# Kernel optimization log

Hardware: AMD Instinct MI355X
Metric: run time of the kernel (lower is better)

The kernel has to match this reference:

```python
import jax, jax.numpy as jnp
import numpy as np

B, N, DIM = 2, 2048, 1024
HEADS, DIM_HEAD = 16, 64
INNER = HEADS * DIM_HEAD  # 1024
SCALE = DIM_HEAD ** -0.5


def setup_inputs() -> dict:
    key = jax.random.key(0)
    ks = jax.random.split(key, 6)
    s = lambda k, shape, fan: jax.random.normal(k, shape, jnp.float32) * (fan ** -0.5)
    return {
        "x": jax.random.normal(ks[0], (B, N, DIM), jnp.float32),
        "similarity": jax.random.normal(ks[1], (B, N), jnp.float32),
        "Wq": s(ks[2], (DIM, INNER), DIM),
        "Wkv": s(ks[3], (DIM, 2 * INNER), DIM),
        "Wo": s(ks[4], (INNER, DIM), INNER),
        "bo": jnp.zeros((DIM,), jnp.float32),
    }


def reference(x, similarity, Wq, Wkv, Wo, bo):
    b, n, _ = x.shape
    h, d = HEADS, DIM_HEAD
    # projections (context = x, self-attention)
    q = (x @ Wq).reshape(b, n, h, d).transpose(0, 2, 1, 3)        # b h n d
    kv = x @ Wkv                                                   # b n 2*inner
    k, v = jnp.split(kv, 2, axis=-1)
    k = k.reshape(b, n, h, d).transpose(0, 2, 1, 3)
    v = v.reshape(b, n, h, d).transpose(0, 2, 1, 3)
    dots = jnp.einsum('bhid,bhjd->bhij', q, k) * SCALE             # b h n n
    # similarity [b,n] -> broadcast as per-query row bias [b,1,n,1]
    dots = dots + similarity[:, None, :, None]
    attn = jax.nn.softmax(dots, axis=-1)
    out = jnp.einsum('bhij,bhjd->bhid', attn, v)                   # b h n d
    out = out.transpose(0, 2, 1, 3).reshape(b, n, h * d)           # b n inner
    return out @ Wo + bo
```

## Files before the change

kernel.cpp:

```cpp
#include <hip/hip_runtime.h>


typedef __attribute__((ext_vector_type(8))) short short8;
typedef __attribute__((ext_vector_type(4))) float float4_;
typedef __attribute__((ext_vector_type(16))) float floatx16;
typedef __attribute__((ext_vector_type(4))) unsigned short ushort4_;

#define MFMA(a, b, c) __builtin_amdgcn_mfma_f32_16x16x32_bf16((a), (b), (c), 0, 0, 0)
#define MFMA32(a, b, c) __builtin_amdgcn_mfma_f32_32x32x16_bf16((a), (b), (c), 0, 0, 0)

static __device__ __forceinline__ unsigned short f2bf(float f) {
    union { float f; unsigned int u; } v; v.f = f;
    unsigned int r = v.u + 0x7FFFu + ((v.u >> 16) & 1u);
    return (unsigned short)(r >> 16);
}

static __device__ __forceinline__ void gld16(const void* g, void* l) {
    __builtin_amdgcn_global_load_lds(
        (__attribute__((address_space(1))) void*)(g),
        (__attribute__((address_space(3))) void*)(l), 16, 0, 0);
}

__global__ __launch_bounds__(256) void prep(
    const float* __restrict__ X, const float* __restrict__ Wq,
    const float* __restrict__ Wkv, const float* __restrict__ Wo,
    unsigned short* __restrict__ xb, unsigned short* __restrict__ Wt,
    unsigned short* __restrict__ Wot)
{
    const int bid = blockIdx.x, t = threadIdx.x;
    if (bid >= 1024) {
        const int b = bid - 1024;
        const float4_* src = (const float4_*)X;
        ushort4_* dst = (ushort4_*)xb;
        #pragma unroll
        for (int g = 0; g < 8; ++g) {
            const int idx = b * 2048 + g * 256 + t;
            float4_ v = src[idx];
            ushort4_ o;
            o[0] = f2bf(v[0]); o[1] = f2bf(v[1]);
            o[2] = f2bf(v[2]); o[3] = f2bf(v[3]);
            dst[idx] = o;
        }
        return;
    }
    __shared__ float tile[64][65];
    const float* src; unsigned short* dst; int N, kt, nt, drow0;
    if (bid < 256)      { src = Wq;  N = 1024; kt = bid & 15;       nt = bid >> 4;       dst = Wt;  drow0 = nt * 64; }
    else if (bid < 768) { src = Wkv; N = 2048; kt = (bid-256) & 15; nt = (bid-256) >> 4; dst = Wt;  drow0 = 1024 + nt * 64; }
    else                { src = Wo;  N = 1024; kt = (bid-768) & 15; nt = (bid-768) >> 4; dst = Wot; drow0 = nt * 64; }
    const int k0 = kt * 64, n0 = nt * 64;
    const int r0 = t >> 6, c = t & 63;
    #pragma unroll
    for (int i = 0; i < 16; ++i) {
        const int r = i * 4 + r0;
        tile[r][c] = src[(size_t)(k0 + r) * N + n0 + c];
    }
    __syncthreads();
    #pragma unroll
    for (int i = 0; i < 16; ++i) {
        const int rn = i * 4 + r0;
        dst[(size_t)(drow0 + rn) * 1024 + k0 + c] = f2bf(tile[c][rn]);
    }
}

__global__ __launch_bounds__(256) void qkv_gemm2(
    const unsigned short* __restrict__ xb, const unsigned short* __restrict__ Wt,
    unsigned short* __restrict__ q_ws, unsigned short* __restrict__ k_ws,
    unsigned short* __restrict__ vt_ws)
{
    __shared__ unsigned short As[128 * 64];
    __shared__ unsigned short Bs[128 * 64];
    const int t = threadIdx.x, wave = t >> 6, lane = t & 63;
    const int L = lane & 15, quad = lane >> 4;
    const int mb = blockIdx.x / 24, nb = blockIdx.x % 24;
    const int m0 = mb * 128, n0 = nb * 128;
    const int wr = wave >> 1, wc = wave & 1;

    float4_ z = {0.f, 0.f, 0.f, 0.f};
    float4_ acc[4][4];
    #pragma unroll
    for (int i = 0; i < 4; ++i)
        #pragma unroll
        for (int j = 0; j < 4; ++j) acc[i][j] = z;

    const unsigned short* gA[4]; const unsigned short* gB[4];
    unsigned short* lA[4]; unsigned short* lB[4];
    #pragma unroll
    for (int j = 0; j < 4; ++j) {
        const int cid = wave * 256 + j * 64 + lane;
        const int row = cid >> 3, pc = cid & 7;
        const int lch = pc ^ (row & 7);
        gA[j] = xb + (size_t)(m0 + row) * 1024 + lch * 8;
        gB[j] = Wt + (size_t)(n0 + row) * 1024 + lch * 8;
        lA[j] = As + wave * 2048 + j * 512;
        lB[j] = Bs + wave * 2048 + j * 512;
    }

    for (int kc = 0; kc < 1024; kc += 64) {
        #pragma unroll
        for (int j = 0; j < 4; ++j) {
            gld16(gA[j] + kc, lA[j]);
            gld16(gB[j] + kc, lB[j]);
        }
        __syncthreads();
        #pragma unroll
        for (int ks = 0; ks < 2; ++ks) {
            short8 af[4], bfr[4];
            #pragma unroll
            for (int mt = 0; mt < 4; ++mt) {
                const int rl = wr * 64 + mt * 16 + L;
                af[mt] = *(const short8*)(As + rl * 64 + (((ks * 4 + quad) ^ (L & 7)) << 3));
            }
            #pragma unroll
            for (int nt = 0; nt < 4; ++nt) {
                const int rl = wc * 64 + nt * 16 + L;
                bfr[nt] = *(const short8*)(Bs + rl * 64 + (((ks * 4 + quad) ^ (L & 7)) << 3));
            }
            #pragma unroll
            for (int mt = 0; mt < 4; ++mt)
                #pragma unroll
                for (int nt = 0; nt < 4; ++nt)
                    acc[mt][nt] = MFMA(af[mt], bfr[nt], acc[mt][nt]);
        }
        __syncthreads();
    }

    const int b = m0 >> 11;
    const int type = n0 >> 10;
    #pragma unroll
    for (int mt = 0; mt < 4; ++mt) {
        const int m = (m0 & 2047) + wr * 64 + mt * 16 + quad * 4;
        #pragma unroll
        for (int nt = 0; nt < 4; ++nt) {
            const int cl = (n0 & 1023) + wc * 64 + nt * 16 + L;
            const int h = cl >> 6, d = cl & 63;
            float4_ v = acc[mt][nt];
            if (type == 0) {
                unsigned short* p = q_ws + ((size_t)(b * 16 + h) * 2048 + m) * 64 + d;
                #pragma unroll
                for (int r = 0; r < 4; ++r) p[(size_t)r * 64] = f2bf(v[r] * 0.18033688011f);
            } else if (type == 1) {
                unsigned short* p = k_ws + ((size_t)(b * 16 + h) * 2048 + m) * 64 + d;
                #pragma unroll
                for (int r = 0; r < 4; ++r) p[(size_t)r * 64] = f2bf(v[r]);
            } else {
                ushort4_ pk;
                pk[0] = f2bf(v[0]); pk[1] = f2bf(v[1]);
                pk[2] = f2bf(v[2]); pk[3] = f2bf(v[3]);
                *(ushort4_*)(vt_ws + ((size_t)(b * 16 + h) * 64 + d) * 2048 + m) = pk;
            }
        }
    }
}

__global__ __launch_bounds__(256) void attn_fwd2(
    const unsigned short* __restrict__ q_ws,
    const unsigned short* __restrict__ k_ws,
    const unsigned short* __restrict__ vt_ws,
    unsigned short* __restrict__ o2)
{
    __shared__ unsigned short k_lds[2][64 * 64];
    __shared__ unsigned short v_lds[2][64 * 64];
    __shared__ unsigned short p_lds[128 * 64];
    const int t = threadIdx.x, wave = t >> 6, lane = t & 63;
    const int l32 = lane & 31, hi = lane >> 5;
    const int bh = blockIdx.x >> 4, qb = blockIdx.x & 15;

    const unsigned short* Kp = k_ws + (size_t)bh * 2048 * 64;
    const unsigned short* Vt = vt_ws + (size_t)bh * 64 * 2048;

    const unsigned short* Qp = q_ws + ((size_t)bh * 2048 + qb * 128 + wave * 32 + l32) * 64;
    short8 qf[4];
    #pragma unroll
    for (int s = 0; s < 4; ++s) qf[s] = *(const short8*)(Qp + hi * 8 + s * 16);

    const int c0 = wave * 64 + lane;
    const int kr0 = c0 >> 3, kl0 = (c0 & 7) ^ (kr0 & 7);
    const int kr1 = kr0 + 32, kl1 = kl0;
    const unsigned short* ks0 = Kp + (size_t)kr0 * 64 + kl0 * 8;
    const unsigned short* ks1 = Kp + (size_t)kr1 * 64 + kl1 * 8;
    const unsigned short* vs0 = Vt + (size_t)kr0 * 2048 + kl0 * 8;
    const unsigned short* vs1 = Vt + (size_t)kr1 * 2048 + kl1 * 8;
    const int dst0 = wave * 512, dst1 = 2048 + wave * 512;

    floatx16 o0 = {0.f}, o1 = {0.f};
    #pragma unroll
    for (int r = 0; r < 16; ++r) { o0[r] = 0.f; o1[r] = 0.f; }
    float lsum[16];
    #pragma unroll
    for (int r = 0; r < 16; ++r) lsum[r] = 0.f;

    gld16(ks0, k_lds[0] + dst0); gld16(ks1, k_lds[0] + dst1);
    gld16(vs0, v_lds[0] + dst0); gld16(vs1, v_lds[0] + dst1);
    __syncthreads();

    const int prow = wave * 32 + l32;
    const int myrow[4] = {0, 1, 2, 3};

    for (int j0 = 0; j0 < 2048; j0 += 64) {
        const int p = (j0 >> 6) & 1;
        if (j0 + 64 < 2048) {
            const int np = p ^ 1;
            gld16(ks0 + (j0 + 64) * 64, k_lds[np] + dst0);
            gld16(ks1 + (j0 + 64) * 64, k_lds[np] + dst1);
            gld16(vs0 + (j0 + 64), v_lds[np] + dst0);
            gld16(vs1 + (j0 + 64), v_lds[np] + dst1);
        }
        const unsigned short* kb = k_lds[p];
        const unsigned short* vb = v_lds[p];

        floatx16 s0 = o0, s1 = o0;
        #pragma unroll
        for (int r = 0; r < 16; ++r) { s0[r] = 0.f; s1[r] = 0.f; }
        #pragma unroll
        for (int s = 0; s < 4; ++s) {
            const int lch = hi + 2 * s;
            short8 k0 = *(const short8*)(kb + l32 * 64 + ((lch ^ (l32 & 7)) << 3));
            short8 k1 = *(const short8*)(kb + (32 + l32) * 64 + ((lch ^ (l32 & 7)) << 3));
            s0 = MFMA32(qf[s], k0, s0);
            s1 = MFMA32(qf[s], k1, s1);
        }

        #pragma unroll
        for (int r = 0; r < 16; ++r) {
            const int row = wave * 32 + (r & 3) + 8 * (r >> 2) + 4 * hi;
            float p0 = __builtin_amdgcn_exp2f(s0[r]);
            float p1 = __builtin_amdgcn_exp2f(s1[r]);
            lsum[r] += p0 + p1;
            union { float f; unsigned int u; } cv0, cv1;
            cv0.f = p0; cv1.f = p1;
            const int ch0 = (l32 >> 3) ^ (row & 7);
            const int ch1 = (4 + (l32 >> 3)) ^ (row & 7);
            p_lds[row * 64 + ch0 * 8 + (l32 & 7)] = (unsigned short)(cv0.u >> 16);
            p_lds[row * 64 + ch1 * 8 + (l32 & 7)] = (unsigned short)(cv1.u >> 16);
        }

        #pragma unroll
        for (int s = 0; s < 4; ++s) {
            const int lch = hi + 2 * s;
            short8 pa = *(const short8*)(p_lds + prow * 64 + ((lch ^ (prow & 7)) << 3));
            short8 v0 = *(const short8*)(vb + l32 * 64 + ((lch ^ (l32 & 7)) << 3));
            short8 v1 = *(const short8*)(vb + (32 + l32) * 64 + ((lch ^ (l32 & 7)) << 3));
            o0 = MFMA32(pa, v0, o0);
            o1 = MFMA32(pa, v1, o1);
        }
        __syncthreads();
    }

    float inv[16];
    #pragma unroll
    for (int r = 0; r < 16; ++r) {
        float l = lsum[r];
        l += __shfl_xor(l, 1); l += __shfl_xor(l, 2);
        l += __shfl_xor(l, 4); l += __shfl_xor(l, 8);
        l += __shfl_xor(l, 16);
        inv[r] = 1.0f / l;
    }
    const int b = bh >> 4, h = bh & 15;
    unsigned short* ob = o2 + ((size_t)b * 2048 + qb * 128 + wave * 32) * 1024 + h * 64;
    #pragma unroll
    for (int r = 0; r < 16; ++r) {
        const int row = (r & 3) + 8 * (r >> 2) + 4 * hi;
        ob[(size_t)row * 1024 + l32]      = f2bf(o0[r] * inv[r]);
        ob[(size_t)row * 1024 + 32 + l32] = f2bf(o1[r] * inv[r]);
    }
}

__global__ __launch_bounds__(256) void out_gemm2(
    const unsigned short* __restrict__ o2, const unsigned short* __restrict__ Wot,
    const float* __restrict__ bo, float* __restrict__ Out)
{
    __shared__ unsigned short As[128 * 64];
    __shared__ unsigned short Bs[64 * 64];
    const int t = threadIdx.x, wave = t >> 6, lane = t & 63;
    const int L = lane & 15, quad = lane >> 4;
    const int mb = blockIdx.x >> 4, nb = blockIdx.x & 15;
    const int m0 = mb * 128, n0 = nb * 64;
    const int wr = wave >> 1, wc = wave & 1;

    float4_ z = {0.f, 0.f, 0.f, 0.f};
    float4_ acc[4][2];
    #pragma unroll
    for (int i = 0; i < 4; ++i)
        #pragma unroll
        for (int j = 0; j < 2; ++j) acc[i][j] = z;

    const unsigned short* gA[4]; unsigned short* lA[4];
    #pragma unroll
    for (int j = 0; j < 4; ++j) {
        const int cid = wave * 256 + j * 64 + lane;
        const int row = cid >> 3, pc = cid & 7;
        gA[j] = o2 + (size_t)(m0 + row) * 1024 + (pc ^ (row & 7)) * 8;
        lA[j] = As + wave * 2048 + j * 512;
    }
    const unsigned short* gB[2]; unsigned short* lB[2];
    #pragma unroll
    for (int j = 0; j < 2; ++j) {
        const int cid = wave * 128 + j * 64 + lane;
        const int row = cid >> 3, pc = cid & 7;
        gB[j] = Wot + (size_t)(n0 + row) * 1024 + (pc ^ (row & 7)) * 8;
        lB[j] = Bs + wave * 1024 + j * 512;
    }

    for (int kc = 0; kc < 1024; kc += 64) {
        #pragma unroll
        for (int j = 0; j < 4; ++j) gld16(gA[j] + kc, lA[j]);
        #pragma unroll
        for (int j = 0; j < 2; ++j) gld16(gB[j] + kc, lB[j]);
        __syncthreads();
        #pragma unroll
        for (int ks = 0; ks < 2; ++ks) {
            short8 af[4], bfr[2];
            #pragma unroll
            for (int mt = 0; mt < 4; ++mt) {
                const int rl = wr * 64 + mt * 16 + L;
                af[mt] = *(const short8*)(As + rl * 64 + (((ks * 4 + quad) ^ (L & 7)) << 3));
            }
            #pragma unroll
            for (int nt = 0; nt < 2; ++nt) {
                const int rl = wc * 32 + nt * 16 + L;
                bfr[nt] = *(const short8*)(Bs + rl * 64 + (((ks * 4 + quad) ^ (L & 7)) << 3));
            }
            #pragma unroll
            for (int mt = 0; mt < 4; ++mt)
                #pragma unroll
                for (int nt = 0; nt < 2; ++nt)
                    acc[mt][nt] = MFMA(af[mt], bfr[nt], acc[mt][nt]);
        }
        __syncthreads();
    }

    #pragma unroll
    for (int mt = 0; mt < 4; ++mt) {
        const int m = m0 + wr * 64 + mt * 16 + quad * 4;
        #pragma unroll
        for (int nt = 0; nt < 2; ++nt) {
            const int c = n0 + wc * 32 + nt * 16 + L;
            const float bias = bo[c];
            #pragma unroll
            for (int r = 0; r < 4; ++r)
                Out[(size_t)(m + r) * 1024 + c] = acc[mt][nt][r] + bias;
        }
    }
}

extern "C" void kernel_launch(void* const* d_in, const int* in_sizes, int n_in,
                              void* d_out, int out_size, void* d_ws, size_t ws_size,
                              hipStream_t stream) {
    const float* x   = (const float*)d_in[0];
    const float* Wq  = (const float*)d_in[2];
    const float* Wkv = (const float*)d_in[3];
    const float* Wo  = (const float*)d_in[4];
    const float* bo  = (const float*)d_in[5];
    float* out = (float*)d_out;

    char* ws = (char*)d_ws;
    const size_t MB = 1024 * 1024;
    unsigned short* xb   = (unsigned short*)(ws);
    unsigned short* o2   = xb;
    unsigned short* Wt   = (unsigned short*)(ws + 8 * MB);
    unsigned short* Wot  = (unsigned short*)(ws + 14 * MB);
    unsigned short* q_ws = (unsigned short*)(ws + 16 * MB);
    unsigned short* k_ws = (unsigned short*)(ws + 24 * MB);
    unsigned short* vt_ws= (unsigned short*)(ws + 32 * MB);

    prep<<<dim3(1536), dim3(256), 0, stream>>>(x, Wq, Wkv, Wo, xb, Wt, Wot);
    qkv_gemm2<<<dim3(768), dim3(256), 0, stream>>>(xb, Wt, q_ws, k_ws, vt_ws);
    attn_fwd2<<<dim3(512), dim3(256), 0, stream>>>(q_ws, k_ws, vt_ws, o2);
    out_gemm2<<<dim3(512), dim3(256), 0, stream>>>(o2, Wot, bo, out);
}
```

Before: 208.2 us.

## Keep attention probabilities in registers by transposing S MFMA operands

The QK^T MFMA now uses K as the A operand and Q as B, so each lane holds score values in an arrangement that can be packed straight into the bf16 A fragment of the PV MFMA. This removes the per-tile round trip of P through LDS (the scattered 16-bit stores and reloads) and reduces row sums to one scalar per lane. V reads become split 8-byte LDS loads that match the permuted key ordering, and row sums are exchanged through a small LDS array at the end. The risk is that the V fragment permutation must match the packed P layout exactly. The ls array is written and read across lanes without a barrier, which relies on lockstep execution within a wave.

Result: faster. 198.1 us (-4.9%).

```diff
diff --git a/kernel.cpp b/kernel.cpp
--- a/kernel.cpp
+++ b/kernel.cpp
@@ -5,6 +5,7 @@
 typedef __attribute__((ext_vector_type(4))) float float4_;
 typedef __attribute__((ext_vector_type(16))) float floatx16;
 typedef __attribute__((ext_vector_type(4))) unsigned short ushort4_;
+typedef __attribute__((ext_vector_type(4))) unsigned int uint4_;
 
 #define MFMA(a, b, c) __builtin_amdgcn_mfma_f32_16x16x32_bf16((a), (b), (c), 0, 0, 0)
 #define MFMA32(a, b, c) __builtin_amdgcn_mfma_f32_32x32x16_bf16((a), (b), (c), 0, 0, 0)
@@ -153,7 +154,7 @@
     }
 }
 
-__global__ __launch_bounds__(256) void attn_fwd2(
+__global__ __launch_bounds__(256) void attn_fwd3(
     const unsigned short* __restrict__ q_ws,
     const unsigned short* __restrict__ k_ws,
     const unsigned short* __restrict__ vt_ws,
@@ -161,7 +162,7 @@
 {
     __shared__ unsigned short k_lds[2][64 * 64];
     __shared__ unsigned short v_lds[2][64 * 64];
-    __shared__ unsigned short p_lds[128 * 64];
+    __shared__ float ls[4][32];
     const int t = threadIdx.x, wave = t >> 6, lane = t & 63;
     const int l32 = lane & 31, hi = lane >> 5;
     const int bh = blockIdx.x >> 4, qb = blockIdx.x & 15;
@@ -176,27 +177,23 @@
 
     const int c0 = wave * 64 + lane;
     const int kr0 = c0 >> 3, kl0 = (c0 & 7) ^ (kr0 & 7);
-    const int kr1 = kr0 + 32, kl1 = kl0;
+    const int kr1 = kr0 + 32;
     const unsigned short* ks0 = Kp + (size_t)kr0 * 64 + kl0 * 8;
-    const unsigned short* ks1 = Kp + (size_t)kr1 * 64 + kl1 * 8;
+    const unsigned short* ks1 = Kp + (size_t)kr1 * 64 + kl0 * 8;
     const unsigned short* vs0 = Vt + (size_t)kr0 * 2048 + kl0 * 8;
-    const unsigned short* vs1 = Vt + (size_t)kr1 * 2048 + kl1 * 8;
+    const unsigned short* vs1 = Vt + (size_t)kr1 * 2048 + kl0 * 8;
     const int dst0 = wave * 512, dst1 = 2048 + wave * 512;
 
-    floatx16 o0 = {0.f}, o1 = {0.f};
+    floatx16 o0, o1;
     #pragma unroll
     for (int r = 0; r < 16; ++r) { o0[r] = 0.f; o1[r] = 0.f; }
-    float lsum[16];
-    #pragma unroll
-    for (int r = 0; r < 16; ++r) lsum[r] = 0.f;
+    float lsum = 0.f;
 
     gld16(ks0, k_lds[0] + dst0); gld16(ks1, k_lds[0] + dst1);
     gld16(vs0, v_lds[0] + dst0); gld16(vs1, v_lds[0] + dst1);
     __syncthreads();
 
-    const int prow = wave * 32 + l32;
-    const int myrow[4] = {0, 1, 2, 3};
-
+    const int sw = l32 & 7;
     for (int j0 = 0; j0 < 2048; j0 += 64) {
         const int p = (j0 >> 6) & 1;
         if (j0 + 64 < 2048) {
@@ -209,53 +206,67 @@
         const unsigned short* kb = k_lds[p];
         const unsigned short* vb = v_lds[p];
 
-        floatx16 s0 = o0, s1 = o0;
+        floatx16 s0, s1;
         #pragma unroll
         for (int r = 0; r < 16; ++r) { s0[r] = 0.f; s1[r] = 0.f; }
         #pragma unroll
         for (int s = 0; s < 4; ++s) {
-            const int lch = hi + 2 * s;
-            short8 k0 = *(const short8*)(kb + l32 * 64 + ((lch ^ (l32 & 7)) << 3));
-            short8 k1 = *(const short8*)(kb + (32 + l32) * 64 + ((lch ^ (l32 & 7)) << 3));
-            s0 = MFMA32(qf[s], k0, s0);
-            s1 = MFMA32(qf[s], k1, s1);
-        }
-
-        #pragma unroll
-        for (int r = 0; r < 16; ++r) {
-            const int row = wave * 32 + (r & 3) + 8 * (r >> 2) + 4 * hi;
-            float p0 = __builtin_amdgcn_exp2f(s0[r]);
-            float p1 = __builtin_amdgcn_exp2f(s1[r]);
-            lsum[r] += p0 + p1;
-            union { float f; unsigned int u; } cv0, cv1;
-            cv0.f = p0; cv1.f = p1;
-            const int ch0 = (l32 >> 3) ^ (row & 7);
-            const int ch1 = (4 + (l32 >> 3)) ^ (row & 7);
-            p_lds[row * 64 + ch0 * 8 + (l32 & 7)] = (unsigned short)(cv0.u >> 16);
-            p_lds[row * 64 + ch1 * 8 + (l32 & 7)] = (unsigned short)(cv1.u >> 16);
-        }
-
-        #pragma unroll
-        for (int s = 0; s < 4; ++s) {
-            const int lch = hi + 2 * s;
-            short8 pa = *(const short8*)(p_lds + prow * 64 + ((lch ^ (prow & 7)) << 3));
-            short8 v0 = *(const short8*)(vb + l32 * 64 + ((lch ^ (l32 & 7)) << 3));
-            short8 v1 = *(const short8*)(vb + (32 + l32) * 64 + ((lch ^ (l32 & 7)) << 3));
-            o0 = MFMA32(pa, v0, o0);
-            o1 = MFMA32(pa, v1, o1);
-        }
-        __syncthreads();
-    }
-
+            const int lch = 2 * s + hi;
+            short8 k0 = *(const short8*)(kb + l32 * 64 + ((lch ^ sw) << 3));
+            short8 k1 = *(const short8*)(kb + (32 + l32) * 64 + ((lch ^ sw) << 3));
+            s0 = MFMA32(k0, qf[s], s0);
+            s1 = MFMA32(k1, qf[s], s1);
+        }
+
+        unsigned int pk0[8], pk1[8];
+        #pragma unroll
+        for (int d = 0; d < 8; ++d) {
+            union { float f; unsigned int u; } a0, b0, a1, b1;
+            a0.f = __builtin_amdgcn_exp2f(s0[2 * d]);
+            b0.f = __builtin_amdgcn_exp2f(s0[2 * d + 1]);
+            a1.f = __builtin_amdgcn_exp2f(s1[2 * d]);
+            b1.f = __builtin_amdgcn_exp2f(s1[2 * d + 1]);
+            lsum += (a0.f + b0.f) + (a1.f + b1.f);
+            pk0[d] = (a0.u >> 16) | (b0.u & 0xFFFF0000u);
+            pk1[d] = (a1.u >> 16) | (b1.u & 0xFFFF0000u);
+        }
+
+        #pragma unroll
+        for (int w = 0; w < 4; ++w) {
+            uint4_ pw;
+            if (w == 0)      { pw[0] = pk0[0]; pw[1] = pk0[1]; pw[2] = pk0[2]; pw[3] = pk0[3]; }
+            else if (w == 1) { pw[0] = pk0[4]; pw[1] = pk0[5]; pw[2] = pk0[6]; pw[3] = pk0[7]; }
+            else if (w == 2) { pw[0] = pk1[0]; pw[1] = pk1[1]; pw[2] = pk1[2]; pw[3] = pk1[3]; }
+            else             { pw[0] = pk1[4]; pw[1] = pk1[5]; pw[2] = pk1[6]; pw[3] = pk1[7]; }
+            short8 pa = *(short8*)&pw;
+
+            const unsigned short* vr0 = vb + l32 * 64;
+            const unsigned short* vr1 = vb + (32 + l32) * 64;
+            const int ca = (((2 * w) ^ sw) << 3) + 4 * hi;
+            const int cb = (((2 * w + 1) ^ sw) << 3) + 4 * hi;
+            ushort4_ va0 = *(const ushort4_*)(vr0 + ca);
+            ushort4_ vb0 = *(const ushort4_*)(vr0 + cb);
+            ushort4_ va1 = *(const ushort4_*)(vr1 + ca);
+            ushort4_ vb1 = *(const ushort4_*)(vr1 + cb);
+            short8 vf0, vf1;
+            #pragma unroll
+            for (int i = 0; i < 4; ++i) {
+                vf0[i] = (short)va0[i]; vf0[4 + i] = (short)vb0[i];
+                vf1[i] = (short)va1[i]; vf1[4 + i] = (short)vb1[i];
+            }
+            o0 = MFMA32(pa, vf0, o0);
+            o1 = MFMA32(pa, vf1, o1);
+        }
+        __syncthreads();
+    }
+
+    float ltot = lsum + __shfl_xor(lsum, 32);
+    ls[wave][l32] = ltot;
     float inv[16];
     #pragma unroll
-    for (int r = 0; r < 16; ++r) {
-        float l = lsum[r];
-        l += __shfl_xor(l, 1); l += __shfl_xor(l, 2);
-        l += __shfl_xor(l, 4); l += __shfl_xor(l, 8);
-        l += __shfl_xor(l, 16);
-        inv[r] = 1.0f / l;
-    }
+    for (int r = 0; r < 16; ++r)
+        inv[r] = 1.0f / ls[wave][(r & 3) + 8 * (r >> 2) + 4 * hi];
+
     const int b = bh >> 4, h = bh & 15;
     unsigned short* ob = o2 + ((size_t)b * 2048 + qb * 128 + wave * 32) * 1024 + h * 64;
     #pragma unroll
@@ -366,6 +377,6 @@
 
     prep<<<dim3(1536), dim3(256), 0, stream>>>(x, Wq, Wkv, Wo, xb, Wt, Wot);
     qkv_gemm2<<<dim3(768), dim3(256), 0, stream>>>(xb, Wt, q_ws, k_ws, vt_ws);
-    attn_fwd2<<<dim3(512), dim3(256), 0, stream>>>(q_ws, k_ws, vt_ws, o2);
+    attn_fwd3<<<dim3(512), dim3(256), 0, stream>>>(q_ws, k_ws, vt_ws, o2);
     out_gemm2<<<dim3(512), dim3(256), 0, stream>>>(o2, Wot, bo, out);
 }
```
